# Kernel tuning notes

Hardware: AMD Instinct MI355X
Metric: run time of the kernel (lower is better)

The kernel has to match this reference:

```python
import jax, jax.numpy as jnp
import numpy as np

N = 100000      # nodes
E = 1200000     # edges
F = 16          # in_cont_dim
EMB = 8         # emb_dim
H = 64          # hidden_dim
NL = 3          # num_layers
NT = 32         # num_func_types


def setup_inputs() -> dict:
    key = jax.random.key(0)
    ks = jax.random.split(key, 10)
    s = lambda k, sh: jax.random.normal(k, sh, jnp.float32) * 0.05
    inp = {}
    inp["x_cont"] = jax.random.normal(ks[0], (N, F), jnp.float32)
    inp["func_type"] = jax.random.randint(ks[1], (N,), 0, NT)
    inp["edge_index"] = jax.random.randint(ks[2], (2, E), 0, N)
    inp["emb_table"] = s(ks[3], (NT, EMB))
    inp["W_in"] = s(ks[4], (F + EMB, H)); inp["b_in"] = jnp.zeros((H,), jnp.float32)
    inp["W_g"] = s(ks[5], (NL, H, H));    inp["b_g"] = jnp.zeros((NL, H), jnp.float32)
    inp["W_o1"] = s(ks[6], (H, H));       inp["b_o1"] = jnp.zeros((H,), jnp.float32)
    inp["W_o2"] = s(ks[7], (H, 1));       inp["b_o2"] = jnp.zeros((1,), jnp.float32)
    return inp


def _gcn_layer(x, src, dst, deg_isq, W, b):
    # PyG GCNConv: h = x W; out_i = sum_{j->i} d_i^-1/2 d_j^-1/2 h_j + d_i^-1 h_i + b
    h = x @ W                                   # [N, H]
    norm = deg_isq[src] * deg_isq[dst]          # [E]
    agg = jax.ops.segment_sum(norm[:, None] * h[src], dst, num_segments=N)
    agg = agg + (deg_isq * deg_isq)[:, None] * h  # self-loop contribution
    return agg + b


def reference(x_cont, func_type, edge_index, emb_table, W_in, b_in,
              W_g, b_g, W_o1, b_o1, W_o2, b_o2):
    src, dst = edge_index[0], edge_index[1]
    # degree with self loops (weight 1), computed at target nodes as in gcn_norm
    deg = 1.0 + jax.ops.segment_sum(jnp.ones((E,), x_cont.dtype), dst, num_segments=N)
    deg_isq = jax.lax.rsqrt(deg)
    x = jnp.concatenate([x_cont, emb_table[func_type]], axis=-1)  # [N, F+EMB]
    x = jax.nn.relu(x @ W_in + b_in)
    for i in range(NL):
        x = jax.nn.relu(_gcn_layer(x, src, dst, deg_isq, W_g[i], b_g[i]))
        # dropout is identity in eval mode
    h = jax.nn.relu(x @ W_o1 + b_o1)
    return (h @ W_o2 + b_o2)[:, 0]  # [N]
```

## Files before the change

kernel.cpp:

```cpp
#include <hip/hip_runtime.h>

#define HD 64
#define FC 16
#define FEMB 8

__device__ __forceinline__ float bfu(unsigned u) { return __uint_as_float(u); }
__device__ __forceinline__ unsigned short f2bf(float f) {
    unsigned u = __float_as_uint(f);
    return (unsigned short)((u + 0x7fffu + ((u >> 16) & 1u)) >> 16);
}

__global__ void k_count_rank(const int* __restrict__ dst, int* __restrict__ cnt,
                             int* __restrict__ rank, int E) {
    int e = blockIdx.x * blockDim.x + threadIdx.x;
    if (e >= E) return;
    rank[e] = atomicAdd(&cnt[dst[e]], 1);
}

__global__ void k_scan1(const int* __restrict__ cnt, int* __restrict__ row_part,
                        int* __restrict__ bsum, float* __restrict__ disq, int n) {
    __shared__ int s[256];
    int t = threadIdx.x;
    int i = blockIdx.x * 256 + t;
    int v = (i < n) ? cnt[i] : 0;
    if (i < n) disq[i] = rsqrtf(1.0f + (float)v);
    s[t] = v;
    __syncthreads();
    for (int off = 1; off < 256; off <<= 1) {
        int a = (t >= off) ? s[t - off] : 0;
        __syncthreads();
        s[t] += a;
        __syncthreads();
    }
    if (i < n) row_part[i] = s[t] - v;
    if (t == 255) bsum[blockIdx.x] = s[255];
}

__global__ void k_scan2(int* __restrict__ bsum, int nb) {
    __shared__ int s[1024];
    int t = threadIdx.x;
    int v = (t < nb) ? bsum[t] : 0;
    s[t] = v;
    __syncthreads();
    for (int off = 1; off < 1024; off <<= 1) {
        int a = (t >= off) ? s[t - off] : 0;
        __syncthreads();
        s[t] += a;
        __syncthreads();
    }
    if (t < nb) bsum[t] = s[t] - v;
}

__global__ void k_scan3(int* __restrict__ row_part, const int* __restrict__ bsum, int n) {
    int stride = gridDim.x * blockDim.x;
    for (int i = blockIdx.x * blockDim.x + threadIdx.x; i < n; i += stride)
        row_part[i] += bsum[i >> 8];
}

__global__ void k_reorder(const int* __restrict__ src, const int* __restrict__ dst,
                          const int* __restrict__ rank, const int* __restrict__ rowst,
                          int* __restrict__ csr, int E) {
    int e = blockIdx.x * blockDim.x + threadIdx.x;
    if (e >= E) return;
    csr[rowst[dst[e]] + rank[e]] = src[e];
}

__global__ void k_input(const float* __restrict__ xc, const int* __restrict__ ft,
                        const float* __restrict__ emb, const float* __restrict__ Win,
                        const float* __restrict__ bin, const float* __restrict__ disq,
                        unsigned short* __restrict__ y, int n) {
    int lane = threadIdx.x & 63;
    int wid  = (blockIdx.x * blockDim.x + threadIdx.x) >> 6;
    if (wid >= n) return;
    float acc = bin[lane];
    const float* xr = xc + (size_t)wid * FC;
#pragma unroll
    for (int k = 0; k < FC; k++)
        acc = fmaf(xr[k], Win[k * HD + lane], acc);
    int t = ft[wid];
    const float* er = emb + (size_t)t * FEMB;
#pragma unroll
    for (int k = 0; k < FEMB; k++)
        acc = fmaf(er[k], Win[(FC + k) * HD + lane], acc);
    y[(size_t)wid * HD + lane] = f2bf(fmaxf(acc, 0.0f) * disq[wid]);
}

__global__ void k_agg(const uint4* __restrict__ y4, const int* __restrict__ csr,
                      const int* __restrict__ rs, const int* __restrict__ deg,
                      const float* __restrict__ disq, float* __restrict__ agg, int n) {
    int lane = threadIdx.x & 63;
    int node = (blockIdx.x * blockDim.x + threadIdx.x) >> 6;
    if (node >= n) return;
    int g = lane >> 3;
    int c = lane & 7;
    int start = rs[node];
    int end   = start + deg[node];
    float di  = disq[node];
    float a0 = 0.f, a1 = 0.f, a2 = 0.f, a3 = 0.f;
    float a4 = 0.f, a5 = 0.f, a6 = 0.f, a7 = 0.f;
    for (int j = start; j < end; j += 16) {
        int e0 = j + g, e1 = j + 8 + g;
        bool ok0 = e0 < end, ok1 = e1 < end;
        int s0 = csr[ok0 ? e0 : j];
        int s1 = csr[ok1 ? e1 : j];
        uint4 v0 = y4[(size_t)s0 * 8 + c];
        uint4 v1 = y4[(size_t)s1 * 8 + c];
        if (ok0) {
            a0 += bfu(v0.x << 16); a1 += bfu(v0.x & 0xffff0000u);
            a2 += bfu(v0.y << 16); a3 += bfu(v0.y & 0xffff0000u);
            a4 += bfu(v0.z << 16); a5 += bfu(v0.z & 0xffff0000u);
            a6 += bfu(v0.w << 16); a7 += bfu(v0.w & 0xffff0000u);
        }
        if (ok1) {
            a0 += bfu(v1.x << 16); a1 += bfu(v1.x & 0xffff0000u);
            a2 += bfu(v1.y << 16); a3 += bfu(v1.y & 0xffff0000u);
            a4 += bfu(v1.z << 16); a5 += bfu(v1.z & 0xffff0000u);
            a6 += bfu(v1.w << 16); a7 += bfu(v1.w & 0xffff0000u);
        }
    }
#define RED8(off) \
    a0 += __shfl_xor(a0, off); a1 += __shfl_xor(a1, off); \
    a2 += __shfl_xor(a2, off); a3 += __shfl_xor(a3, off); \
    a4 += __shfl_xor(a4, off); a5 += __shfl_xor(a5, off); \
    a6 += __shfl_xor(a6, off); a7 += __shfl_xor(a7, off);
    RED8(8) RED8(16) RED8(32)
#undef RED8
    if (g == 0) {
        uint4 sv = y4[(size_t)node * 8 + c];
        a0 += bfu(sv.x << 16); a1 += bfu(sv.x & 0xffff0000u);
        a2 += bfu(sv.y << 16); a3 += bfu(sv.y & 0xffff0000u);
        a4 += bfu(sv.z << 16); a5 += bfu(sv.z & 0xffff0000u);
        a6 += bfu(sv.w << 16); a7 += bfu(sv.w & 0xffff0000u);
        float4* ap = (float4*)(agg + (size_t)node * HD + c * 8);
        float4 o1 = {di * a0, di * a1, di * a2, di * a3};
        float4 o2 = {di * a4, di * a5, di * a6, di * a7};
        ap[0] = o1;
        ap[1] = o2;
    }
}

__global__ __launch_bounds__(256, 4)
void k_mm(const float* __restrict__ x, const float* __restrict__ W,
          const float* __restrict__ b, const float* __restrict__ disq,
          unsigned short* __restrict__ yo, int n) {
    __shared__ float4 ws4[64][16];
    __shared__ float4 xs4[64][17];
    int tid = threadIdx.x;
    int node0 = blockIdx.x * 64;

    for (int i = tid; i < 1024; i += 256)
        ws4[i >> 4][i & 15] = ((const float4*)W)[i];
    for (int i = tid; i < 1024; i += 256) {
        int nn = i >> 4, k4 = i & 15;
        int row = node0 + nn; if (row >= n) row = n - 1;
        xs4[nn][k4] = ((const float4*)(x + (size_t)row * HD))[k4];
    }
    __syncthreads();

    int tc4 = tid & 15;
    int tn  = (tid >> 4) * 4;
    float4 ac0 = {0,0,0,0}, ac1 = {0,0,0,0}, ac2 = {0,0,0,0}, ac3 = {0,0,0,0};

#pragma unroll 4
    for (int k4 = 0; k4 < 16; k4++) {
        float4 w0 = ws4[k4 * 4 + 0][tc4];
        float4 w1 = ws4[k4 * 4 + 1][tc4];
        float4 w2 = ws4[k4 * 4 + 2][tc4];
        float4 w3 = ws4[k4 * 4 + 3][tc4];
#pragma unroll
        for (int i = 0; i < 4; i++) {
            float4 xv = xs4[tn + i][k4];
            float4* ac = (i == 0) ? &ac0 : (i == 1) ? &ac1 : (i == 2) ? &ac2 : &ac3;
            ac->x = fmaf(xv.x, w0.x, ac->x); ac->y = fmaf(xv.x, w0.y, ac->y);
            ac->z = fmaf(xv.x, w0.z, ac->z); ac->w = fmaf(xv.x, w0.w, ac->w);
            ac->x = fmaf(xv.y, w1.x, ac->x); ac->y = fmaf(xv.y, w1.y, ac->y);
            ac->z = fmaf(xv.y, w1.z, ac->z); ac->w = fmaf(xv.y, w1.w, ac->w);
            ac->x = fmaf(xv.z, w2.x, ac->x); ac->y = fmaf(xv.z, w2.y, ac->y);
            ac->z = fmaf(xv.z, w2.z, ac->z); ac->w = fmaf(xv.z, w2.w, ac->w);
            ac->x = fmaf(xv.w, w3.x, ac->x); ac->y = fmaf(xv.w, w3.y, ac->y);
            ac->z = fmaf(xv.w, w3.z, ac->z); ac->w = fmaf(xv.w, w3.w, ac->w);
        }
    }

    float4 bb = ((const float4*)b)[tc4];
    float4 accs[4] = {ac0, ac1, ac2, ac3};
#pragma unroll
    for (int i = 0; i < 4; i++) {
        int row = node0 + tn + i;
        if (row < n) {
            float dq = disq[row];
            ushort4 o;
            o.x = f2bf(fmaxf(accs[i].x + bb.x, 0.0f) * dq);
            o.y = f2bf(fmaxf(accs[i].y + bb.y, 0.0f) * dq);
            o.z = f2bf(fmaxf(accs[i].z + bb.z, 0.0f) * dq);
            o.w = f2bf(fmaxf(accs[i].w + bb.w, 0.0f) * dq);
            *(ushort4*)(yo + (size_t)row * HD + tc4 * 4) = o;
        }
    }
}

__global__ __launch_bounds__(256, 4)
void k_mm_head(const float* __restrict__ x, const float* __restrict__ W,
               const float* __restrict__ b, const float* __restrict__ W1,
               const float* __restrict__ b1, const float* __restrict__ W2,
               const float* __restrict__ b2, float* __restrict__ out, int n) {
    __shared__ float4 ws4[64][16];
    __shared__ float4 xs4[64][17];
    int tid = threadIdx.x;
    int node0 = blockIdx.x * 64;

    for (int i = tid; i < 1024; i += 256)
        ws4[i >> 4][i & 15] = ((const float4*)W)[i];
    for (int i = tid; i < 1024; i += 256) {
        int nn = i >> 4, k4 = i & 15;
        int row = node0 + nn; if (row >= n) row = n - 1;
        xs4[nn][k4] = ((const float4*)(x + (size_t)row * HD))[k4];
    }
    __syncthreads();

    int tc4 = tid & 15;
    int tn  = (tid >> 4) * 4;

    float4 ac0 = {0,0,0,0}, ac1 = {0,0,0,0}, ac2 = {0,0,0,0}, ac3 = {0,0,0,0};
#pragma unroll 4
    for (int k4 = 0; k4 < 16; k4++) {
        float4 w0 = ws4[k4 * 4 + 0][tc4];
        float4 w1 = ws4[k4 * 4 + 1][tc4];
        float4 w2 = ws4[k4 * 4 + 2][tc4];
        float4 w3 = ws4[k4 * 4 + 3][tc4];
#pragma unroll
        for (int i = 0; i < 4; i++) {
            float4 xv = xs4[tn + i][k4];
            float4* ac = (i == 0) ? &ac0 : (i == 1) ? &ac1 : (i == 2) ? &ac2 : &ac3;
            ac->x = fmaf(xv.x, w0.x, ac->x); ac->y = fmaf(xv.x, w0.y, ac->y);
            ac->z = fmaf(xv.x, w0.z, ac->z); ac->w = fmaf(xv.x, w0.w, ac->w);
            ac->x = fmaf(xv.y, w1.x, ac->x); ac->y = fmaf(xv.y, w1.y, ac->y);
            ac->z = fmaf(xv.y, w1.z, ac->z); ac->w = fmaf(xv.y, w1.w, ac->w);
            ac->x = fmaf(xv.z, w2.x, ac->x); ac->y = fmaf(xv.z, w2.y, ac->y);
            ac->z = fmaf(xv.z, w2.z, ac->z); ac->w = fmaf(xv.z, w2.w, ac->w);
            ac->x = fmaf(xv.w, w3.x, ac->x); ac->y = fmaf(xv.w, w3.y, ac->y);
            ac->z = fmaf(xv.w, w3.z, ac->z); ac->w = fmaf(xv.w, w3.w, ac->w);
        }
    }
    __syncthreads();

    {
        float4 bb = ((const float4*)b)[tc4];
        float4 accs[4] = {ac0, ac1, ac2, ac3};
#pragma unroll
        for (int i = 0; i < 4; i++) {
            float4 o;
            o.x = fmaxf(accs[i].x + bb.x, 0.0f);
            o.y = fmaxf(accs[i].y + bb.y, 0.0f);
            o.z = fmaxf(accs[i].z + bb.z, 0.0f);
            o.w = fmaxf(accs[i].w + bb.w, 0.0f);
            xs4[tn + i][tc4] = o;
        }
    }
    for (int i = tid; i < 1024; i += 256)
        ws4[i >> 4][i & 15] = ((const float4*)W1)[i];
    __syncthreads();

    float4 bc0 = {0,0,0,0}, bc1 = {0,0,0,0}, bc2 = {0,0,0,0}, bc3 = {0,0,0,0};
#pragma unroll 4
    for (int k4 = 0; k4 < 16; k4++) {
        float4 w0 = ws4[k4 * 4 + 0][tc4];
        float4 w1 = ws4[k4 * 4 + 1][tc4];
        float4 w2 = ws4[k4 * 4 + 2][tc4];
        float4 w3 = ws4[k4 * 4 + 3][tc4];
#pragma unroll
        for (int i = 0; i < 4; i++) {
            float4 xv = xs4[tn + i][k4];
            float4* ac = (i == 0) ? &bc0 : (i == 1) ? &bc1 : (i == 2) ? &bc2 : &bc3;
            ac->x = fmaf(xv.x, w0.x, ac->x); ac->y = fmaf(xv.x, w0.y, ac->y);
            ac->z = fmaf(xv.x, w0.z, ac->z); ac->w = fmaf(xv.x, w0.w, ac->w);
            ac->x = fmaf(xv.y, w1.x, ac->x); ac->y = fmaf(xv.y, w1.y, ac->y);
            ac->z = fmaf(xv.y, w1.z, ac->z); ac->w = fmaf(xv.y, w1.w, ac->w);
            ac->x = fmaf(xv.z, w2.x, ac->x); ac->y = fmaf(xv.z, w2.y, ac->y);
            ac->z = fmaf(xv.z, w2.z, ac->z); ac->w = fmaf(xv.z, w2.w, ac->w);
            ac->x = fmaf(xv.w, w3.x, ac->x); ac->y = fmaf(xv.w, w3.y, ac->y);
            ac->z = fmaf(xv.w, w3.z, ac->z); ac->w = fmaf(xv.w, w3.w, ac->w);
        }
    }

    float4 b1v = ((const float4*)b1)[tc4];
    float4 w2v = ((const float4*)W2)[tc4];
    float b2v  = b2[0];
    float4 bcs[4] = {bc0, bc1, bc2, bc3};
#pragma unroll
    for (int i = 0; i < 4; i++) {
        float s = fmaxf(bcs[i].x + b1v.x, 0.0f) * w2v.x
                + fmaxf(bcs[i].y + b1v.y, 0.0f) * w2v.y
                + fmaxf(bcs[i].z + b1v.z, 0.0f) * w2v.z
                + fmaxf(bcs[i].w + b1v.w, 0.0f) * w2v.w;
        s += __shfl_xor(s, 1);
        s += __shfl_xor(s, 2);
        s += __shfl_xor(s, 4);
        s += __shfl_xor(s, 8);
        int row = node0 + tn + i;
        if (tc4 == 0 && row < n) out[row] = s + b2v;
    }
}

extern "C" void kernel_launch(void* const* d_in, const int* in_sizes, int n_in,
                              void* d_out, int out_size, void* d_ws, size_t ws_size,
                              hipStream_t stream) {
    const float* x_cont = (const float*)d_in[0];
    const int*   ftyp   = (const int*)d_in[1];
    const int*   eidx   = (const int*)d_in[2];
    const float* emb    = (const float*)d_in[3];
    const float* W_in   = (const float*)d_in[4];
    const float* b_in   = (const float*)d_in[5];
    const float* W_g    = (const float*)d_in[6];
    const float* b_g    = (const float*)d_in[7];
    const float* W_o1   = (const float*)d_in[8];
    const float* b_o1   = (const float*)d_in[9];
    const float* W_o2   = (const float*)d_in[10];
    const float* b_o2   = (const float*)d_in[11];
    float* out = (float*)d_out;

    const int n = in_sizes[1];
    const int E = in_sizes[2] / 2;
    const int* src = eidx;
    const int* dst = eidx + E;

    char* p = (char*)d_ws;
    auto alloc = [&](size_t bytes) {
        char* r = p;
        p += (bytes + 255) & ~(size_t)255;
        return r;
    };
    int*   cnt   = (int*)  alloc((size_t)n * 4);
    float* disq  = (float*)alloc((size_t)n * 4);
    int*   rowst = (int*)  alloc((size_t)n * 4);
    int*   bsum  = (int*)  alloc(4096);
    int*   rank  = (int*)  alloc((size_t)E * 4);
    int*   csr   = (int*)  alloc((size_t)E * 4);
    unsigned short* y16 = (unsigned short*)alloc((size_t)n * HD * 2);
    float* agg   = (float*)alloc((size_t)n * HD * 4);

    hipMemsetAsync(cnt, 0, (size_t)n * 4, stream);

    dim3 blk(256);
    const int nb1   = (n + 255) / 256;
    const int nb_e  = (E + 255) / 256;
    const int nb_nw = (n + 3) / 4;
    const int nb_t  = (n + 63) / 64;

    k_count_rank<<<nb_e, blk, 0, stream>>>(dst, cnt, rank, E);
    k_scan1<<<nb1, blk, 0, stream>>>(cnt, rowst, bsum, disq, n);
    k_scan2<<<1, 1024, 0, stream>>>(bsum, nb1);
    k_scan3<<<512, blk, 0, stream>>>(rowst, bsum, n);
    k_reorder<<<nb_e, blk, 0, stream>>>(src, dst, rank, rowst, csr, E);
    k_input<<<nb_nw, blk, 0, stream>>>(x_cont, ftyp, emb, W_in, b_in, disq, y16, n);

    for (int L = 0; L < 2; L++) {
        k_agg<<<nb_nw, blk, 0, stream>>>((const uint4*)y16, csr, rowst, cnt, disq, agg, n);
        k_mm<<<nb_t, blk, 0, stream>>>(agg, W_g + (size_t)L * HD * HD,
                                       b_g + (size_t)L * HD, disq, y16, n);
    }
    k_agg<<<nb_nw, blk, 0, stream>>>((const uint4*)y16, csr, rowst, cnt, disq, agg, n);
    k_mm_head<<<nb_t, blk, 0, stream>>>(agg, W_g + (size_t)2 * HD * HD,
                                        b_g + (size_t)2 * HD,
                                        W_o1, b_o1, W_o2, b_o2, out, n);
}
```

Baseline: 319.7 us.

## Pack degree counters to 16-bit, fold scan fixup into consumers, drop scan3

Degree counts are packed two per 32-bit word with 16-bit atomic increments, which halves the counter array and the memset, and each count thread handles two edges. The third scan kernel is removed: consumers add the block offset (bsum) to the partial row start themselves. The CSR scatter uses nontemporal stores. This trades a few extra loads and bit ops in the aggregation kernels for one fewer launch and less counter traffic, and it assumes no node has 65536 or more incoming edges.

After: 344.6 us. +7.8%, slower.

```diff
diff --git a/kernel.cpp b/kernel.cpp
--- a/kernel.cpp
+++ b/kernel.cpp
@@ -10,20 +10,34 @@
     return (unsigned short)((u + 0x7fffu + ((u >> 16) & 1u)) >> 16);
 }
 
-__global__ void k_count_rank(const int* __restrict__ dst, int* __restrict__ cnt,
-                             int* __restrict__ rank, int E) {
-    int e = blockIdx.x * blockDim.x + threadIdx.x;
-    if (e >= E) return;
-    rank[e] = atomicAdd(&cnt[dst[e]], 1);
-}
-
-__global__ void k_scan1(const int* __restrict__ cnt, int* __restrict__ row_part,
+__global__ void k_count_rank(const int* __restrict__ dst, unsigned* __restrict__ cnt32,
+                             int* __restrict__ rank, int E, int Eh) {
+    int t = blockIdx.x * blockDim.x + threadIdx.x;
+    if (t < Eh) {
+        int d0 = dst[t];
+        int d1v = (t + Eh < E) ? dst[t + Eh] : -1;
+        unsigned sh0 = (d0 & 1) << 4;
+        unsigned old0 = atomicAdd(&cnt32[d0 >> 1], 1u << sh0);
+        if (d1v >= 0) {
+            unsigned sh1 = (d1v & 1) << 4;
+            unsigned old1 = atomicAdd(&cnt32[d1v >> 1], 1u << sh1);
+            rank[t + Eh] = (old1 >> sh1) & 0xffffu;
+        }
+        rank[t] = (old0 >> sh0) & 0xffffu;
+    }
+}
+
+__global__ void k_scan1(const unsigned* __restrict__ cnt32, int* __restrict__ row_part,
                         int* __restrict__ bsum, float* __restrict__ disq, int n) {
     __shared__ int s[256];
     int t = threadIdx.x;
     int i = blockIdx.x * 256 + t;
-    int v = (i < n) ? cnt[i] : 0;
-    if (i < n) disq[i] = rsqrtf(1.0f + (float)v);
+    int v = 0;
+    if (i < n) {
+        unsigned w = cnt32[i >> 1];
+        v = (int)((w >> ((i & 1) << 4)) & 0xffffu);
+        disq[i] = rsqrtf(1.0f + (float)v);
+    }
     s[t] = v;
     __syncthreads();
     for (int off = 1; off < 256; off <<= 1) {
@@ -51,18 +65,14 @@
     if (t < nb) bsum[t] = s[t] - v;
 }
 
-__global__ void k_scan3(int* __restrict__ row_part, const int* __restrict__ bsum, int n) {
-    int stride = gridDim.x * blockDim.x;
-    for (int i = blockIdx.x * blockDim.x + threadIdx.x; i < n; i += stride)
-        row_part[i] += bsum[i >> 8];
-}
-
 __global__ void k_reorder(const int* __restrict__ src, const int* __restrict__ dst,
-                          const int* __restrict__ rank, const int* __restrict__ rowst,
-                          int* __restrict__ csr, int E) {
+                          const int* __restrict__ rank, const int* __restrict__ row_part,
+                          const int* __restrict__ bsum, int* __restrict__ csr, int E) {
     int e = blockIdx.x * blockDim.x + threadIdx.x;
     if (e >= E) return;
-    csr[rowst[dst[e]] + rank[e]] = src[e];
+    int d = dst[e];
+    int pos = row_part[d] + bsum[d >> 8] + rank[e];
+    __builtin_nontemporal_store(src[e], &csr[pos]);
 }
 
 __global__ void k_input(const float* __restrict__ xc, const int* __restrict__ ft,
@@ -86,15 +96,17 @@
 }
 
 __global__ void k_agg(const uint4* __restrict__ y4, const int* __restrict__ csr,
-                      const int* __restrict__ rs, const int* __restrict__ deg,
+                      const int* __restrict__ row_part, const int* __restrict__ bsum,
+                      const unsigned* __restrict__ cnt32,
                       const float* __restrict__ disq, float* __restrict__ agg, int n) {
     int lane = threadIdx.x & 63;
     int node = (blockIdx.x * blockDim.x + threadIdx.x) >> 6;
     if (node >= n) return;
     int g = lane >> 3;
     int c = lane & 7;
-    int start = rs[node];
-    int end   = start + deg[node];
+    int start = row_part[node] + bsum[node >> 8];
+    int deg   = (int)((cnt32[node >> 1] >> ((node & 1) << 4)) & 0xffffu);
+    int end   = start + deg;
     float di  = disq[node];
     float a0 = 0.f, a1 = 0.f, a2 = 0.f, a3 = 0.f;
     float a4 = 0.f, a5 = 0.f, a6 = 0.f, a7 = 0.f;
@@ -330,36 +342,39 @@
         p += (bytes + 255) & ~(size_t)255;
         return r;
     };
-    int*   cnt   = (int*)  alloc((size_t)n * 4);
-    float* disq  = (float*)alloc((size_t)n * 4);
-    int*   rowst = (int*)  alloc((size_t)n * 4);
-    int*   bsum  = (int*)  alloc(4096);
-    int*   rank  = (int*)  alloc((size_t)E * 4);
-    int*   csr   = (int*)  alloc((size_t)E * 4);
+    unsigned* cnt32    = (unsigned*)alloc(((size_t)n / 2 + 1) * 4);
+    float*    disq     = (float*)   alloc((size_t)n * 4);
+    int*      row_part = (int*)     alloc((size_t)n * 4);
+    int*      bsum     = (int*)     alloc(4096);
+    int*      rank     = (int*)     alloc((size_t)E * 4);
+    int*      csr      = (int*)     alloc((size_t)E * 4);
     unsigned short* y16 = (unsigned short*)alloc((size_t)n * HD * 2);
-    float* agg   = (float*)alloc((size_t)n * HD * 4);
-
-    hipMemsetAsync(cnt, 0, (size_t)n * 4, stream);
+    float*    agg      = (float*)   alloc((size_t)n * HD * 4);
+
+    hipMemsetAsync(cnt32, 0, ((size_t)n / 2 + 1) * 4, stream);
 
     dim3 blk(256);
     const int nb1   = (n + 255) / 256;
+    const int Eh    = (E + 1) / 2;
+    const int nb_c  = (Eh + 255) / 256;
     const int nb_e  = (E + 255) / 256;
     const int nb_nw = (n + 3) / 4;
     const int nb_t  = (n + 63) / 64;
 
-    k_count_rank<<<nb_e, blk, 0, stream>>>(dst, cnt, rank, E);
-    k_scan1<<<nb1, blk, 0, stream>>>(cnt, rowst, bsum, disq, n);
+    k_count_rank<<<nb_c, blk, 0, stream>>>(dst, cnt32, rank, E, Eh);
+    k_scan1<<<nb1, blk, 0, stream>>>(cnt32, row_part, bsum, disq, n);
     k_scan2<<<1, 1024, 0, stream>>>(bsum, nb1);
-    k_scan3<<<512, blk, 0, stream>>>(rowst, bsum, n);
-    k_reorder<<<nb_e, blk, 0, stream>>>(src, dst, rank, rowst, csr, E);
+    k_reorder<<<nb_e, blk, 0, stream>>>(src, dst, rank, row_part, bsum, csr, E);
     k_input<<<nb_nw, blk, 0, stream>>>(x_cont, ftyp, emb, W_in, b_in, disq, y16, n);
 
     for (int L = 0; L < 2; L++) {
-        k_agg<<<nb_nw, blk, 0, stream>>>((const uint4*)y16, csr, rowst, cnt, disq, agg, n);
+        k_agg<<<nb_nw, blk, 0, stream>>>((const uint4*)y16, csr, row_part, bsum,
+                                         cnt32, disq, agg, n);
         k_mm<<<nb_t, blk, 0, stream>>>(agg, W_g + (size_t)L * HD * HD,
                                        b_g + (size_t)L * HD, disq, y16, n);
     }
-    k_agg<<<nb_nw, blk, 0, stream>>>((const uint4*)y16, csr, rowst, cnt, disq, agg, n);
+    k_agg<<<nb_nw, blk, 0, stream>>>((const uint4*)y16, csr, row_part, bsum,
+                                     cnt32, disq, agg, n);
     k_mm_head<<<nb_t, blk, 0, stream>>>(agg, W_g + (size_t)2 * HD * HD,
                                         b_g + (size_t)2 * HD,
                                         W_o1, b_o1, W_o2, b_o2, out, n);
```

## Fuse scan fixup into consumers, merge reorder with input projection, vectorize counting

Applied to the files above, without the earlier changes.

The separate scan-fixup kernel is removed: consumers now add the block prefix from bsum on the fly, in both the reorder and aggregation kernels. The CSR reorder and the input-projection kernel are merged into one launch that splits work by block index, and the CSR write uses a nontemporal store. Edge counting handles four edges per thread with int4 loads and stores. The aggregation loop skips the second eight-edge gather when no edges remain, which avoids wasted loads for low-degree nodes. Together these cut kernel launches and memory passes, at the cost of an extra bsum load per access and branchier code.

After: 340.7 us. 1.07x slower.

```diff
diff --git a/kernel.cpp b/kernel.cpp
--- a/kernel.cpp
+++ b/kernel.cpp
@@ -12,9 +12,19 @@
 
 __global__ void k_count_rank(const int* __restrict__ dst, int* __restrict__ cnt,
                              int* __restrict__ rank, int E) {
-    int e = blockIdx.x * blockDim.x + threadIdx.x;
-    if (e >= E) return;
-    rank[e] = atomicAdd(&cnt[dst[e]], 1);
+    int t = blockIdx.x * blockDim.x + threadIdx.x;
+    int base = t * 4;
+    if (base + 4 <= E) {
+        int4 d = *(const int4*)(dst + base);
+        int r0 = atomicAdd(&cnt[d.x], 1);
+        int r1 = atomicAdd(&cnt[d.y], 1);
+        int r2 = atomicAdd(&cnt[d.z], 1);
+        int r3 = atomicAdd(&cnt[d.w], 1);
+        *(int4*)(rank + base) = make_int4(r0, r1, r2, r3);
+    } else {
+        for (int e = base; e < E; e++)
+            rank[e] = atomicAdd(&cnt[dst[e]], 1);
+    }
 }
 
 __global__ void k_scan1(const int* __restrict__ cnt, int* __restrict__ row_part,
@@ -51,71 +61,77 @@
     if (t < nb) bsum[t] = s[t] - v;
 }
 
-__global__ void k_scan3(int* __restrict__ row_part, const int* __restrict__ bsum, int n) {
-    int stride = gridDim.x * blockDim.x;
-    for (int i = blockIdx.x * blockDim.x + threadIdx.x; i < n; i += stride)
-        row_part[i] += bsum[i >> 8];
-}
-
-__global__ void k_reorder(const int* __restrict__ src, const int* __restrict__ dst,
-                          const int* __restrict__ rank, const int* __restrict__ rowst,
-                          int* __restrict__ csr, int E) {
-    int e = blockIdx.x * blockDim.x + threadIdx.x;
-    if (e >= E) return;
-    csr[rowst[dst[e]] + rank[e]] = src[e];
-}
-
-__global__ void k_input(const float* __restrict__ xc, const int* __restrict__ ft,
-                        const float* __restrict__ emb, const float* __restrict__ Win,
-                        const float* __restrict__ bin, const float* __restrict__ disq,
-                        unsigned short* __restrict__ y, int n) {
-    int lane = threadIdx.x & 63;
-    int wid  = (blockIdx.x * blockDim.x + threadIdx.x) >> 6;
-    if (wid >= n) return;
-    float acc = bin[lane];
-    const float* xr = xc + (size_t)wid * FC;
-#pragma unroll
-    for (int k = 0; k < FC; k++)
-        acc = fmaf(xr[k], Win[k * HD + lane], acc);
-    int t = ft[wid];
-    const float* er = emb + (size_t)t * FEMB;
-#pragma unroll
-    for (int k = 0; k < FEMB; k++)
-        acc = fmaf(er[k], Win[(FC + k) * HD + lane], acc);
-    y[(size_t)wid * HD + lane] = f2bf(fmaxf(acc, 0.0f) * disq[wid]);
+__global__ void k_reorder_input(const int* __restrict__ src, const int* __restrict__ dst,
+                                const int* __restrict__ rank, const int* __restrict__ row_part,
+                                const int* __restrict__ bsum, int* __restrict__ csr, int E,
+                                int nb_e,
+                                const float* __restrict__ xc, const int* __restrict__ ft,
+                                const float* __restrict__ emb, const float* __restrict__ Win,
+                                const float* __restrict__ bin, const float* __restrict__ disq,
+                                unsigned short* __restrict__ y, int n) {
+    int b = blockIdx.x;
+    if (b < nb_e) {
+        int e = b * 256 + threadIdx.x;
+        if (e < E) {
+            int d = dst[e];
+            int pos = row_part[d] + bsum[d >> 8] + rank[e];
+            __builtin_nontemporal_store(src[e], &csr[pos]);
+        }
+    } else {
+        int lane = threadIdx.x & 63;
+        int wid  = (((b - nb_e) * 256 + (int)threadIdx.x) >> 6);
+        if (wid >= n) return;
+        float acc = bin[lane];
+        const float* xr = xc + (size_t)wid * FC;
+#pragma unroll
+        for (int k = 0; k < FC; k++)
+            acc = fmaf(xr[k], Win[k * HD + lane], acc);
+        int t = ft[wid];
+        const float* er = emb + (size_t)t * FEMB;
+#pragma unroll
+        for (int k = 0; k < FEMB; k++)
+            acc = fmaf(er[k], Win[(FC + k) * HD + lane], acc);
+        y[(size_t)wid * HD + lane] = f2bf(fmaxf(acc, 0.0f) * disq[wid]);
+    }
 }
 
 __global__ void k_agg(const uint4* __restrict__ y4, const int* __restrict__ csr,
-                      const int* __restrict__ rs, const int* __restrict__ deg,
+                      const int* __restrict__ row_part, const int* __restrict__ bsum,
+                      const int* __restrict__ cnt,
                       const float* __restrict__ disq, float* __restrict__ agg, int n) {
     int lane = threadIdx.x & 63;
     int node = (blockIdx.x * blockDim.x + threadIdx.x) >> 6;
     if (node >= n) return;
     int g = lane >> 3;
     int c = lane & 7;
-    int start = rs[node];
-    int end   = start + deg[node];
+    int start = row_part[node] + bsum[node >> 8];
+    int deg   = cnt[node];
+    int end   = start + deg;
     float di  = disq[node];
     float a0 = 0.f, a1 = 0.f, a2 = 0.f, a3 = 0.f;
     float a4 = 0.f, a5 = 0.f, a6 = 0.f, a7 = 0.f;
     for (int j = start; j < end; j += 16) {
-        int e0 = j + g, e1 = j + 8 + g;
-        bool ok0 = e0 < end, ok1 = e1 < end;
+        int e0 = j + g;
+        bool ok0 = e0 < end;
         int s0 = csr[ok0 ? e0 : j];
-        int s1 = csr[ok1 ? e1 : j];
         uint4 v0 = y4[(size_t)s0 * 8 + c];
-        uint4 v1 = y4[(size_t)s1 * 8 + c];
         if (ok0) {
             a0 += bfu(v0.x << 16); a1 += bfu(v0.x & 0xffff0000u);
             a2 += bfu(v0.y << 16); a3 += bfu(v0.y & 0xffff0000u);
             a4 += bfu(v0.z << 16); a5 += bfu(v0.z & 0xffff0000u);
             a6 += bfu(v0.w << 16); a7 += bfu(v0.w & 0xffff0000u);
         }
-        if (ok1) {
-            a0 += bfu(v1.x << 16); a1 += bfu(v1.x & 0xffff0000u);
-            a2 += bfu(v1.y << 16); a3 += bfu(v1.y & 0xffff0000u);
-            a4 += bfu(v1.z << 16); a5 += bfu(v1.z & 0xffff0000u);
-            a6 += bfu(v1.w << 16); a7 += bfu(v1.w & 0xffff0000u);
+        if (j + 8 < end) {
+            int e1 = j + 8 + g;
+            bool ok1 = e1 < end;
+            int s1 = csr[ok1 ? e1 : j];
+            uint4 v1 = y4[(size_t)s1 * 8 + c];
+            if (ok1) {
+                a0 += bfu(v1.x << 16); a1 += bfu(v1.x & 0xffff0000u);
+                a2 += bfu(v1.y << 16); a3 += bfu(v1.y & 0xffff0000u);
+                a4 += bfu(v1.z << 16); a5 += bfu(v1.z & 0xffff0000u);
+                a6 += bfu(v1.w << 16); a7 += bfu(v1.w & 0xffff0000u);
+            }
         }
     }
 #define RED8(off) \
@@ -330,36 +346,39 @@
         p += (bytes + 255) & ~(size_t)255;
         return r;
     };
-    int*   cnt   = (int*)  alloc((size_t)n * 4);
-    float* disq  = (float*)alloc((size_t)n * 4);
-    int*   rowst = (int*)  alloc((size_t)n * 4);
-    int*   bsum  = (int*)  alloc(4096);
-    int*   rank  = (int*)  alloc((size_t)E * 4);
-    int*   csr   = (int*)  alloc((size_t)E * 4);
+    int*      cnt      = (int*)  alloc((size_t)n * 4);
+    float*    disq     = (float*)alloc((size_t)n * 4);
+    int*      row_part = (int*)  alloc((size_t)n * 4);
+    int*      bsum     = (int*)  alloc(4096);
+    int*      rank     = (int*)  alloc((size_t)E * 4);
+    int*      csr      = (int*)  alloc((size_t)E * 4);
     unsigned short* y16 = (unsigned short*)alloc((size_t)n * HD * 2);
-    float* agg   = (float*)alloc((size_t)n * HD * 4);
+    float*    agg      = (float*)alloc((size_t)n * HD * 4);
 
     hipMemsetAsync(cnt, 0, (size_t)n * 4, stream);
 
     dim3 blk(256);
     const int nb1   = (n + 255) / 256;
+    const int nb_c  = (E / 4 + 255) / 256;
     const int nb_e  = (E + 255) / 256;
     const int nb_nw = (n + 3) / 4;
     const int nb_t  = (n + 63) / 64;
 
-    k_count_rank<<<nb_e, blk, 0, stream>>>(dst, cnt, rank, E);
-    k_scan1<<<nb1, blk, 0, stream>>>(cnt, rowst, bsum, disq, n);
+    k_count_rank<<<nb_c, blk, 0, stream>>>(dst, cnt, rank, E);
+    k_scan1<<<nb1, blk, 0, stream>>>(cnt, row_part, bsum, disq, n);
     k_scan2<<<1, 1024, 0, stream>>>(bsum, nb1);
-    k_scan3<<<512, blk, 0, stream>>>(rowst, bsum, n);
-    k_reorder<<<nb_e, blk, 0, stream>>>(src, dst, rank, rowst, csr, E);
-    k_input<<<nb_nw, blk, 0, stream>>>(x_cont, ftyp, emb, W_in, b_in, disq, y16, n);
+    k_reorder_input<<<nb_e + nb_nw, blk, 0, stream>>>(
+        src, dst, rank, row_part, bsum, csr, E, nb_e,
+        x_cont, ftyp, emb, W_in, b_in, disq, y16, n);
 
     for (int L = 0; L < 2; L++) {
-        k_agg<<<nb_nw, blk, 0, stream>>>((const uint4*)y16, csr, rowst, cnt, disq, agg, n);
+        k_agg<<<nb_nw, blk, 0, stream>>>((const uint4*)y16, csr, row_part, bsum,
+                                         cnt, disq, agg, n);
         k_mm<<<nb_t, blk, 0, stream>>>(agg, W_g + (size_t)L * HD * HD,
                                        b_g + (size_t)L * HD, disq, y16, n);
     }
-    k_agg<<<nb_nw, blk, 0, stream>>>((const uint4*)y16, csr, rowst, cnt, disq, agg, n);
+    k_agg<<<nb_nw, blk, 0, stream>>>((const uint4*)y16, csr, row_part, bsum,
+                                     cnt, disq, agg, n);
     k_mm_head<<<nb_t, blk, 0, stream>>>(agg, W_g + (size_t)2 * HD * HD,
                                         b_g + (size_t)2 * HD,
                                         W_o1, b_o1, W_o2, b_o2, out, n);
```
